# Kernel tuning notes

Hardware: AMD Instinct MI355X
Metric: run time of the kernel (lower is better)

The kernel has to match this reference:

```python
import jax, jax.numpy as jnp
import numpy as np

B, T, E, A = 128, 1024, 512, 512   # batch, encoder time, embed_size, attention units
D = 512                            # memory (encoder output) dim
H = E // 2                         # prenet out / decoder GRU cell size
OUT = 80 * 5                       # n_mels * r


def _gru(x, h, W, U, b_i, b_r):
    # Keras GRU (reset_after=True): separate input/recurrent biases.
    n = h.shape[-1]
    gi = x @ W + b_i                       # [B, 3n]
    gr = h @ U + b_r                       # [B, 3n]
    z = jax.nn.sigmoid(gi[:, :n] + gr[:, :n])
    r = jax.nn.sigmoid(gi[:, n:2 * n] + gr[:, n:2 * n])
    c = jnp.tanh(gi[:, 2 * n:] + r * gr[:, 2 * n:])
    return z * h + (1.0 - z) * c


def setup_inputs() -> dict:
    key = jax.random.key(0)
    ks = jax.random.split(key, 40)
    s = 0.02
    w = lambda i, shape: jax.random.normal(ks[i], shape, dtype=jnp.float32) * s
    inp = {
        'inputs': jax.random.normal(ks[0], (B, OUT), dtype=jnp.float32),
        'prev_attn_h': jax.random.normal(ks[1], (B, E), dtype=jnp.float32) * 0.1,
        'prev_dec_h1': jax.random.normal(ks[2], (B, H), dtype=jnp.float32) * 0.1,
        'prev_dec_h2': jax.random.normal(ks[3], (B, H), dtype=jnp.float32) * 0.1,
        'prev_alignments': jax.nn.softmax(jax.random.normal(ks[4], (B, T), dtype=jnp.float32)),
        'memory': jax.random.normal(ks[5], (B, T, D), dtype=jnp.float32),
        'memory_mask': jnp.ones((B, T), dtype=bool),
        # prenet: Dense(E) relu, Dense(E//2) relu (dropout off at eval)
        'Wp1': w(6, (OUT, E)), 'bp1': jnp.zeros((E,), jnp.float32),
        'Wp2': w(7, (E, H)), 'bp2': jnp.zeros((H,), jnp.float32),
        # Bahdanau attention: v^T tanh(Wq q + Wk m)
        'Wq': w(8, (E, A)), 'Wk': w(9, (D, A)), 'v_attn': w(10, (A,)),
        # attention_layer Dense(E) on previous context
        'Wa': w(11, (D, E)), 'ba': jnp.zeros((E,), jnp.float32),
        # attention GRU: input = prenet(H) ++ prev_attention(E)
        'Wg': w(12, (H + E, 3 * E)), 'Ug': w(13, (E, 3 * E)),
        'bg_i': jnp.zeros((3 * E,), jnp.float32), 'bg_r': jnp.zeros((3 * E,), jnp.float32),
        # stacked decoder GRU cells (E//2 each): input = attn_h(E) ++ context(D)
        'Wd1': w(14, (E + D, 3 * H)), 'Ud1': w(15, (H, 3 * H)),
        'bd1_i': jnp.zeros((3 * H,), jnp.float32), 'bd1_r': jnp.zeros((3 * H,), jnp.float32),
        'Wd2': w(16, (H, 3 * H)), 'Ud2': w(17, (H, 3 * H)),
        'bd2_i': jnp.zeros((3 * H,), jnp.float32), 'bd2_r': jnp.zeros((3 * H,), jnp.float32),
        # projection to mel frame(s)
        'Wo': w(18, (H, OUT)), 'bo': jnp.zeros((OUT,), jnp.float32),
    }
    return inp


def reference(inputs, prev_attn_h, prev_dec_h1, prev_dec_h2, prev_alignments,
              memory, memory_mask,
              Wp1, bp1, Wp2, bp2,
              Wq, Wk, v_attn, Wa, ba,
              Wg, Ug, bg_i, bg_r,
              Wd1, Ud1, bd1_i, bd1_r,
              Wd2, Ud2, bd2_i, bd2_r,
              Wo, bo):
    # 1) context from previous alignments, projected by attention_layer
    prev_ctx = jnp.einsum('bt,btd->bd', prev_alignments, memory)       # [B, D]
    prev_attention = prev_ctx @ Wa + ba                                # [B, E]
    # 2) prenet (eval mode: dropout disabled)
    pre = jax.nn.relu(inputs @ Wp1 + bp1)
    pre = jax.nn.relu(pre @ Wp2 + bp2)                                 # [B, H]
    # 3) attention GRU (single step)
    attn_in = jnp.concatenate([pre, prev_attention], axis=-1)          # [B, H+E]
    attn_h = _gru(attn_in, prev_attn_h, Wg, Ug, bg_i, bg_r)            # [B, E]
    # 4) Bahdanau attention with new query
    score = jnp.einsum('bta,a->bt', jnp.tanh((attn_h @ Wq)[:, None, :] + jnp.einsum('btd,da->bta', memory, Wk)), v_attn)
    score = jnp.where(memory_mask, score, jnp.float32(-1e9))
    alignments = jax.nn.softmax(score, axis=-1)                        # [B, T]
    context = jnp.einsum('bt,btd->bd', alignments, memory)             # [B, D]
    # 5) stacked decoder GRU cells
    dec_in = jnp.concatenate([attn_h, context], axis=-1)               # [B, E+D]
    h1 = _gru(dec_in, prev_dec_h1, Wd1, Ud1, bd1_i, bd1_r)             # [B, H]
    h2 = _gru(h1, prev_dec_h2, Wd2, Ud2, bd2_i, bd2_r)                 # [B, H]
    # 6) projection to mel frame(s), keep the time axis like the TF model
    final_outputs = (h2 @ Wo + bo)[:, None, :]                         # [B, 1, OUT]
    return final_outputs
```

## Files before the change

kernel.cpp:

```cpp
#include <hip/hip_runtime.h>
#include <cstdint>
#include <cstddef>

constexpr int NB = 128, NT = 1024, NE = 512, NA = 512, ND = 512, NH = 256, NOUT = 400;

typedef __bf16 bf16x8 __attribute__((ext_vector_type(8)));
typedef float f32x4 __attribute__((ext_vector_type(4)));

__device__ __forceinline__ float bf2f(uint16_t u) { return __uint_as_float(((uint32_t)u) << 16); }
__device__ __forceinline__ uint16_t f2bf(float f) {
  uint32_t u = __float_as_uint(f);
  u += 0x7fffu + ((u >> 16) & 1u);
  return (uint16_t)(u >> 16);
}
__device__ __forceinline__ float lo16(uint32_t u) { return __uint_as_float(u << 16); }
__device__ __forceinline__ float hi16(uint32_t u) { return __uint_as_float(u & 0xffff0000u); }
__device__ __forceinline__ float sigmoidf_(float x) { return 1.0f / (1.0f + __expf(-x)); }
__device__ __forceinline__ float tanhf_(float x) { float e = __expf(2.0f * x); return 1.0f - 2.0f / (e + 1.0f); }

__global__ void detect_k(const void* __restrict__ mem, int* __restrict__ flag) {
  __shared__ int red[256];
  int cnt = 0;
  for (int i = threadIdx.x; i < 16384; i += 256) {
    float x = bf2f(((const uint16_t*)mem)[i]);
    float ax = fabsf(x);
    if (!(ax < 100.0f)) cnt++;
  }
  red[threadIdx.x] = cnt;
  __syncthreads();
  for (int s = 128; s > 0; s >>= 1) {
    if (threadIdx.x < s) red[threadIdx.x] += red[threadIdx.x + s];
    __syncthreads();
  }
  if (threadIdx.x == 0) flag[0] = (red[0] < 64) ? 1 : 0;
}

constexpr int NSEG = 27;
struct ConvTab {
  const void* src[NSEG];
  float* dst[NSEG];
  int n[NSEG];
};

__global__ void prep_k(ConvTab t, const int* __restrict__ flag,
                       const void* __restrict__ Wk, uint16_t* __restrict__ WkTf,
                       float* __restrict__ zbase, int zcount) {
  const int y = blockIdx.y;
  const int isb = *flag;
  if (y < NSEG) {
    const int n = t.n[y];
    float* d = t.dst[y];
    if (isb) {
      const uint16_t* p = (const uint16_t*)t.src[y];
      for (int i = blockIdx.x * 256 + threadIdx.x; i < n; i += 64 * 256) d[i] = bf2f(p[i]);
    } else {
      const float* p = (const float*)t.src[y];
      for (int i = blockIdx.x * 256 + threadIdx.x; i < n; i += 64 * 256) d[i] = p[i];
    }
  } else if (y == NSEG) {
    float4* p = (float4*)zbase;
    const int n4 = zcount >> 2;
    for (int i = blockIdx.x * 256 + threadIdx.x; i < n4; i += 64 * 256)
      p[i] = float4{0.f, 0.f, 0.f, 0.f};
  } else {
    for (int idx = blockIdx.x * 256 + threadIdx.x; idx < 32768; idx += 64 * 256) {
      const int lane = idx & 63;
      const int ks = (idx >> 6) & 15;
      const int tt = (idx >> 10) & 3;
      const int ag = idx >> 12;
      const int a = ag * 64 + tt * 16 + (lane & 15);
      const int k0 = ks * 32 + (lane >> 4) * 8;
      uint16_t tmp[8];
      if (isb) {
        const uint16_t* w = (const uint16_t*)Wk;
#pragma unroll
        for (int j = 0; j < 8; ++j) tmp[j] = w[(size_t)(k0 + j) * NA + a];
      } else {
        const float* w = (const float*)Wk;
#pragma unroll
        for (int j = 0; j < 8; ++j) tmp[j] = f2bf(w[(size_t)(k0 + j) * NA + a]);
      }
      *(uint4*)(WkTf + (size_t)idx * 8) = *(const uint4*)tmp;
    }
  }
}

__global__ __launch_bounds__(256) void ctx_k(const int* __restrict__ flagp,
                                             const float* __restrict__ align,
                                             const void* __restrict__ mem,
                                             float* __restrict__ out) {
  const int b = blockIdx.x, tc = blockIdx.y, tid = threadIdx.x;
  const int t0 = tc * 256;
  float ax = 0.f, ay = 0.f;
  if (*flagp) {
    const uint32_t* memu = (const uint32_t*)mem;
    for (int t = t0; t < t0 + 256; ++t) {
      float a = align[b * NT + t];
      uint32_t m = memu[(size_t)(b * NT + t) * (ND / 2) + tid];
      ax = fmaf(a, lo16(m), ax);
      ay = fmaf(a, hi16(m), ay);
    }
  } else {
    const float2* memf = (const float2*)mem;
    for (int t = t0; t < t0 + 256; ++t) {
      float a = align[b * NT + t];
      float2 m = memf[(size_t)(b * NT + t) * (ND / 2) + tid];
      ax = fmaf(a, m.x, ax);
      ay = fmaf(a, m.y, ay);
    }
  }
  atomicAdd(&out[b * ND + 2 * tid], ax);
  atomicAdd(&out[b * ND + 2 * tid + 1], ay);
}

struct GJob {
  const float* X1; const float* X2; const float* W; const float* bias; float* out;
  int K1, K2, N, relu, mode, nb_n, ksplit, kper;
};
struct GLevel { GJob j[4]; };

__global__ __launch_bounds__(256) void gemm_lvl(GLevel L, const int* __restrict__ flagp,
                                                void* __restrict__ dout) {
  const GJob J = L.j[blockIdx.y];
  int bx = blockIdx.x;
  if (bx >= J.nb_n * 2 * J.ksplit) return;
  const int kc = bx % J.ksplit; bx /= J.ksplit;
  const int mb = bx & 1; const int nb = bx >> 1;
  const int K = J.K1 + J.K2;
  const int n0 = nb * 64, m0 = mb * 64;
  const int kbeg = kc * J.kper, kend = kc * J.kper + J.kper;

  __shared__ float Xs[32][66];
  __shared__ float Ws[32][68];
  const int tid = threadIdx.x;
  const int tx = tid & 15, ty = tid >> 4;
  float acc[4][4] = {};

  for (int kt = kbeg; kt < kend; kt += 32) {
    __syncthreads();
    {
      const int m = tid >> 2;
      const int kk = (tid & 3) * 8;
      const float* Xrow1 = J.X1 + (size_t)(m0 + m) * J.K1;
      const float* Xrow2 = J.X2 ? J.X2 + (size_t)(m0 + m) * J.K2 : nullptr;
#pragma unroll
      for (int h = 0; h < 2; ++h) {
        const int kg = kt + kk + h * 4;
        float4 val = {0.f, 0.f, 0.f, 0.f};
        if (kg < K)
          val = (kg < J.K1) ? *(const float4*)(Xrow1 + kg)
                            : *(const float4*)(Xrow2 + (kg - J.K1));
        Xs[kk + h * 4 + 0][m] = val.x;
        Xs[kk + h * 4 + 1][m] = val.y;
        Xs[kk + h * 4 + 2][m] = val.z;
        Xs[kk + h * 4 + 3][m] = val.w;
      }
    }
    {
      const int kr = tid >> 3, nc = (tid & 7) * 8;
      const int k = kt + kr;
#pragma unroll
      for (int h = 0; h < 2; ++h) {
        const int n = n0 + nc + h * 4;
        float4 val = {0.f, 0.f, 0.f, 0.f};
        if (k < K && n < J.N) val = *(const float4*)(J.W + (size_t)k * J.N + n);
        *(float4*)&Ws[kr][nc + h * 4] = val;
      }
    }
    __syncthreads();
#pragma unroll 8
    for (int k = 0; k < 32; ++k) {
      const float4 av = *(const float4*)&Xs[k][ty * 4];
      const float4 bv = *(const float4*)&Ws[k][tx * 4];
      const float aa[4] = {av.x, av.y, av.z, av.w};
      const float bb[4] = {bv.x, bv.y, bv.z, bv.w};
#pragma unroll
      for (int i = 0; i < 4; ++i)
#pragma unroll
        for (int j = 0; j < 4; ++j) acc[i][j] = fmaf(aa[i], bb[j], acc[i][j]);
    }
  }

  const int isb = (J.mode == 1) ? *flagp : 0;
#pragma unroll
  for (int i = 0; i < 4; ++i) {
    const int m = m0 + ty * 4 + i;
#pragma unroll
    for (int j = 0; j < 4; ++j) {
      const int c = n0 + tx * 4 + j;
      if (c >= J.N) continue;
      float r = acc[i][j];
      if (J.ksplit > 1) {
        if (kc == 0 && J.bias) r += J.bias[c];
        atomicAdd(&J.out[(size_t)m * J.N + c], r);
      } else {
        if (J.bias) r += J.bias[c];
        if (J.relu) r = fmaxf(r, 0.f);
        if (J.mode == 1) {
          if (isb) ((uint16_t*)dout)[(size_t)m * J.N + c] = f2bf(r);
          else     ((float*)dout)[(size_t)m * J.N + c] = r;
        } else {
          J.out[(size_t)m * J.N + c] = r;
        }
      }
    }
  }
}

__global__ void gru_k(const float* __restrict__ gi, const float* __restrict__ gr,
                      const float* __restrict__ hprev, float* __restrict__ hout, int n) {
  const int i = blockIdx.x * 256 + threadIdx.x;
  if (i >= NB * n) return;
  const int b = i / n, c = i % n;
  const float* gib = gi + (size_t)b * 3 * n;
  const float* grb = gr + (size_t)b * 3 * n;
  float z = sigmoidf_(gib[c] + grb[c]);
  float r = sigmoidf_(gib[n + c] + grb[n + c]);
  float cc = tanhf_(gib[2 * n + c] + r * grb[2 * n + c]);
  float h = hprev[i];
  hout[i] = z * h + (1.0f - z) * cc;
}

__global__ __launch_bounds__(256) void score_mfma_k(const int* __restrict__ flagp,
                                                    const void* __restrict__ mem,
                                                    const uint16_t* __restrict__ WkTf,
                                                    const float* __restrict__ q,
                                                    const float* __restrict__ v,
                                                    float* __restrict__ score) {
  __shared__ uint16_t memS[64 * 512];
  const int tid = threadIdx.x;
  const int row0 = blockIdx.x * 64;
  const int b = row0 >> 10;
  const int lane = tid & 63, wid = tid >> 6;
  const int quad = lane >> 4;
  const int r15 = lane & 15;

  if (*flagp) {
    const uint16_t* m16 = (const uint16_t*)mem;
#pragma unroll
    for (int it = 0; it < 16; ++it) {
      const int idx = it * 256 + tid;
      const int r = idx >> 6, c8 = (idx & 63) << 3;
      uint4 val = *(const uint4*)(m16 + (size_t)(row0 + r) * ND + c8);
      *(uint4*)&memS[r * 512 + (c8 ^ ((r & 7) << 3))] = val;
    }
  } else {
    const float* m32 = (const float*)mem;
#pragma unroll
    for (int it = 0; it < 32; ++it) {
      const int idx = it * 256 + tid;
      const int r = idx >> 7, c4 = (idx & 127) << 2;
      float4 val = *(const float4*)(m32 + (size_t)(row0 + r) * ND + c4);
      uint2 packed;
      packed.x = (uint32_t)f2bf(val.x) | ((uint32_t)f2bf(val.y) << 16);
      packed.y = (uint32_t)f2bf(val.z) | ((uint32_t)f2bf(val.w) << 16);
      const int col = (((c4 >> 3) ^ (r & 7)) << 3) + (c4 & 7);
      *(uint2*)&memS[r * 512 + col] = packed;
    }
  }
  __syncthreads();

  float part[4] = {0.f, 0.f, 0.f, 0.f};

#pragma unroll
  for (int agi = 0; agi < 2; ++agi) {
    const int ag = wid * 2 + agi;
    f32x4 acc[4][4] = {};
    const uint16_t* agbase = WkTf + (size_t)ag * 32768 + lane * 8;
    for (int ks = 0; ks < 16; ++ks) {
      const uint16_t* p = agbase + ks * 512;
      bf16x8 af0 = *(const bf16x8*)(p);
      bf16x8 af1 = *(const bf16x8*)(p + 8192);
      bf16x8 af2 = *(const bf16x8*)(p + 16384);
      bf16x8 af3 = *(const bf16x8*)(p + 24576);
#pragma unroll
      for (int rt = 0; rt < 4; ++rt) {
        const int lr = rt * 16 + r15;
        const bf16x8 bfrag =
            *(const bf16x8*)&memS[lr * 512 + ((((ks << 2) + quad) ^ (lr & 7)) << 3)];
        acc[rt][0] = __builtin_amdgcn_mfma_f32_16x16x32_bf16(af0, bfrag, acc[rt][0], 0, 0, 0);
        acc[rt][1] = __builtin_amdgcn_mfma_f32_16x16x32_bf16(af1, bfrag, acc[rt][1], 0, 0, 0);
        acc[rt][2] = __builtin_amdgcn_mfma_f32_16x16x32_bf16(af2, bfrag, acc[rt][2], 0, 0, 0);
        acc[rt][3] = __builtin_amdgcn_mfma_f32_16x16x32_bf16(af3, bfrag, acc[rt][3], 0, 0, 0);
      }
    }
    const int a_base = ag * 64 + quad * 4;
#pragma unroll
    for (int rt = 0; rt < 4; ++rt)
#pragma unroll
      for (int t = 0; t < 4; ++t)
#pragma unroll
        for (int r = 0; r < 4; ++r) {
          const int a = a_base + t * 16 + r;
          part[rt] = fmaf(v[a], tanhf_(acc[rt][t][r] + q[b * NA + a]), part[rt]);
        }
  }

#pragma unroll
  for (int rt = 0; rt < 4; ++rt) {
    part[rt] += __shfl_xor(part[rt], 16, 64);
    part[rt] += __shfl_xor(part[rt], 32, 64);
  }
  __syncthreads();
  float* red = (float*)memS;
  if (lane < 16) {
#pragma unroll
    for (int rt = 0; rt < 4; ++rt) red[wid * 64 + rt * 16 + lane] = part[rt];
  }
  __syncthreads();
  if (tid < 64) score[row0 + tid] = red[tid] + red[64 + tid] + red[128 + tid] + red[192 + tid];
}

__global__ __launch_bounds__(256) void softmax_k(const float* __restrict__ score,
                                                 float* __restrict__ align) {
  __shared__ float red[256];
  const int b = blockIdx.x, tid = threadIdx.x;
  float vals[4];
  float m = -1e30f;
#pragma unroll
  for (int j = 0; j < 4; ++j) {
    vals[j] = score[b * NT + j * 256 + tid];
    m = fmaxf(m, vals[j]);
  }
  red[tid] = m;
  __syncthreads();
  for (int s = 128; s > 0; s >>= 1) {
    if (tid < s) red[tid] = fmaxf(red[tid], red[tid + s]);
    __syncthreads();
  }
  m = red[0];
  __syncthreads();
  float sum = 0.f;
#pragma unroll
  for (int j = 0; j < 4; ++j) {
    vals[j] = __expf(vals[j] - m);
    sum += vals[j];
  }
  red[tid] = sum;
  __syncthreads();
  for (int s = 128; s > 0; s >>= 1) {
    if (tid < s) red[tid] += red[tid + s];
    __syncthreads();
  }
  const float inv = 1.0f / red[0];
#pragma unroll
  for (int j = 0; j < 4; ++j) align[b * NT + j * 256 + tid] = vals[j] * inv;
}

extern "C" void kernel_launch(void* const* d_in, const int* in_sizes, int n_in,
                              void* d_out, int out_size, void* d_ws, size_t ws_size,
                              hipStream_t stream) {
  const void* mem = d_in[5];

  int* flagp = (int*)d_ws;
  float* ws = (float*)d_ws + 16;
  float* prev_ctx = ws;
  float* context  = prev_ctx + NB * ND;
  float* qbuf     = context + NB * ND;
  float* prevatt  = qbuf + NB * NA;
  float* gi_g     = prevatt + NB * NE;
  float* gr_g     = gi_g + NB * 3 * NE;
  float* gi_d     = gr_g + NB * 3 * NE;
  float* gr_d     = gi_d + NB * 3 * NH;
  float* gi2      = gr_d + NB * 3 * NH;
  float* gr2      = gi2 + NB * 3 * NH;
  const int zcount = 2 * NB * ND + NB * NA + NB * NE + 2 * NB * 3 * NE + 4 * NB * 3 * NH;
  float* score    = gr2 + NB * 3 * NH;
  float* align    = score + NB * NT;
  float* pre1     = align + NB * NT;
  float* pre2     = pre1 + NB * NE;
  float* attn_h   = pre2 + NB * NH;
  float* h1       = attn_h + NB * NE;
  float* h2       = h1 + NB * NH;
  float* inputs_f = h2 + NB * NH;
  float* pah_f    = inputs_f + NB * NOUT;
  float* pd1_f    = pah_f + NB * NE;
  float* pd2_f    = pd1_f + NB * NH;
  float* palign_f = pd2_f + NB * NH;
  float* wf = palign_f + NB * NT;
  float* Wp1f = wf;                 float* bp1f = Wp1f + 400 * 512;
  float* Wp2f = bp1f + 512;         float* bp2f = Wp2f + 512 * 256;
  float* Wqf  = bp2f + 256;         float* vf   = Wqf + 512 * 512;
  float* Waf  = vf + 512;           float* baf  = Waf + 512 * 512;
  float* Wgf  = baf + 512;          float* Ugf  = Wgf + 768 * 1536;
  float* bgif = Ugf + 512 * 1536;   float* bgrf = bgif + 1536;
  float* Wd1f = bgrf + 1536;        float* Ud1f = Wd1f + 1024 * 768;
  float* bd1if = Ud1f + 256 * 768;  float* bd1rf = bd1if + 768;
  float* Wd2f = bd1rf + 768;        float* Ud2f = Wd2f + 256 * 768;
  float* bd2if = Ud2f + 256 * 768;  float* bd2rf = bd2if + 768;
  float* Wof  = bd2rf + 768;        float* bof  = Wof + 256 * 400;
  uint16_t* WkTf = (uint16_t*)(bof + 400);

  detect_k<<<dim3(1), 256, 0, stream>>>(mem, flagp);

  ConvTab tab;
  const int srcidx[NSEG] = {0, 1, 2, 3, 4, 7, 8, 9, 10, 11, 13, 14, 15, 16, 17, 18, 19,
                            20, 21, 22, 23, 24, 25, 26, 27, 28, 29};
  float* dsts[NSEG] = {inputs_f, pah_f, pd1_f, pd2_f, palign_f,
                       Wp1f, bp1f, Wp2f, bp2f, Wqf, vf, Waf, baf,
                       Wgf, Ugf, bgif, bgrf, Wd1f, Ud1f, bd1if, bd1rf,
                       Wd2f, Ud2f, bd2if, bd2rf, Wof, bof};
  for (int s = 0; s < NSEG; ++s) {
    tab.src[s] = d_in[srcidx[s]];
    tab.dst[s] = dsts[s];
    tab.n[s] = in_sizes[srcidx[s]];
  }
  prep_k<<<dim3(64, NSEG + 2), 256, 0, stream>>>(tab, flagp, d_in[12], WkTf, prev_ctx, zcount);

  ctx_k<<<dim3(NB, 4), 256, 0, stream>>>(flagp, palign_f, mem, prev_ctx);

  auto J = [](const float* X1, int K1, const float* X2, int K2, const float* W,
              const float* bias, float* out, int N, int relu, int mode, int nb_n,
              int ksplit, int kper) {
    GJob j; j.X1 = X1; j.X2 = X2; j.W = W; j.bias = bias; j.out = out;
    j.K1 = K1; j.K2 = K2; j.N = N; j.relu = relu; j.mode = mode;
    j.nb_n = nb_n; j.ksplit = ksplit; j.kper = kper; return j;
  };

  GLevel L1{};
  L1.j[0] = J(inputs_f, NOUT, nullptr, 0, Wp1f, bp1f, pre1, NE, 1, 0, 8, 1, 400);
  L1.j[1] = J(pah_f, NE, nullptr, 0, Ugf, bgrf, gr_g, 3 * NE, 0, 0, 24, 2, 256);
  L1.j[2] = J(pd1_f, NH, nullptr, 0, Ud1f, bd1rf, gr_d, 3 * NH, 0, 0, 12, 1, 256);
  L1.j[3] = J(pd2_f, NH, nullptr, 0, Ud2f, bd2rf, gr2, 3 * NH, 0, 0, 12, 1, 256);
  gemm_lvl<<<dim3(96, 4), 256, 0, stream>>>(L1, flagp, d_out);
  GLevel L2{};
  L2.j[0] = J(prev_ctx, ND, nullptr, 0, Waf, baf, prevatt, NE, 0, 0, 8, 2, 256);
  L2.j[1] = J(pre1, NE, nullptr, 0, Wp2f, bp2f, pre2, NH, 1, 0, 4, 1, 512);
  gemm_lvl<<<dim3(32, 2), 256, 0, stream>>>(L2, flagp, d_out);
  GLevel L3{};
  L3.j[0] = J(pre2, NH, prevatt, NE, Wgf, bgif, gi_g, 3 * NE, 0, 0, 24, 3, 256);
  gemm_lvl<<<dim3(144, 1), 256, 0, stream>>>(L3, flagp, d_out);
  gru_k<<<dim3(NB * NE / 256), 256, 0, stream>>>(gi_g, gr_g, pah_f, attn_h, NE);
  GLevel L4{};
  L4.j[0] = J(attn_h, NE, nullptr, 0, Wqf, nullptr, qbuf, NA, 0, 0, 8, 2, 256);
  gemm_lvl<<<dim3(32, 1), 256, 0, stream>>>(L4, flagp, d_out);
  score_mfma_k<<<dim3(NB * NT / 64), 256, 0, stream>>>(flagp, mem, WkTf, qbuf, vf, score);
  softmax_k<<<dim3(NB), 256, 0, stream>>>(score, align);
  ctx_k<<<dim3(NB, 4), 256, 0, stream>>>(flagp, align, mem, context);
  GLevel L5{};
  L5.j[0] = J(attn_h, NE, context, ND, Wd1f, bd1if, gi_d, 3 * NH, 0, 0, 12, 4, 256);
  gemm_lvl<<<dim3(96, 1), 256, 0, stream>>>(L5, flagp, d_out);
  gru_k<<<dim3(NB * NH / 256), 256, 0, stream>>>(gi_d, gr_d, pd1_f, h1, NH);
  GLevel L6{};
  L6.j[0] = J(h1, NH, nullptr, 0, Wd2f, bd2if, gi2, 3 * NH, 0, 0, 12, 1, 256);
  gemm_lvl<<<dim3(24, 1), 256, 0, stream>>>(L6, flagp, d_out);
  gru_k<<<dim3(NB * NH / 256), 256, 0, stream>>>(gi2, gr2, pd2_f, h2, NH);
  GLevel L7{};
  L7.j[0] = J(h2, NH, nullptr, 0, Wof, bof, nullptr, NOUT, 0, 1, 7, 1, 256);
  gemm_lvl<<<dim3(14, 1), 256, 0, stream>>>(L7, flagp, d_out);
}
```

Baseline: 893.0 us.

## Fuse all decoder stages into one cooperative persistent kernel with grid syncs

Replaces the chain of about twenty separate kernel launches (detect, prep, context, GEMM levels, GRU, score, softmax, context) with a single cooperative kernel. The stages are separated by grid-wide barriers, and tiles are distributed over a persistent grid sized from occupancy. It also overlaps the previous-context reduction with weight conversion, skips the fp32 copy of the previous alignments, and software-prefetches the Wk fragments in the MFMA score loop. The aim is to remove launch and inter-kernel gaps, at the cost of grid.sync overhead and a fixed grid that may underuse the GPU in some phases. The prev_ctx reduction now runs on only 128 blocks over the full time axis.

```diff
diff --git a/kernel.cpp b/kernel.cpp
--- a/kernel.cpp
+++ b/kernel.cpp
@@ -1,6 +1,9 @@
 #include <hip/hip_runtime.h>
+#include <hip/hip_cooperative_groups.h>
 #include <cstdint>
 #include <cstddef>
+
+namespace cg = cooperative_groups;
 
 constexpr int NB = 128, NT = 1024, NE = 512, NA = 512, ND = 512, NH = 256, NOUT = 400;
 
@@ -18,120 +21,38 @@
 __device__ __forceinline__ float sigmoidf_(float x) { return 1.0f / (1.0f + __expf(-x)); }
 __device__ __forceinline__ float tanhf_(float x) { float e = __expf(2.0f * x); return 1.0f - 2.0f / (e + 1.0f); }
 
-__global__ void detect_k(const void* __restrict__ mem, int* __restrict__ flag) {
-  __shared__ int red[256];
-  int cnt = 0;
-  for (int i = threadIdx.x; i < 16384; i += 256) {
-    float x = bf2f(((const uint16_t*)mem)[i]);
-    float ax = fabsf(x);
-    if (!(ax < 100.0f)) cnt++;
-  }
-  red[threadIdx.x] = cnt;
-  __syncthreads();
-  for (int s = 128; s > 0; s >>= 1) {
-    if (threadIdx.x < s) red[threadIdx.x] += red[threadIdx.x + s];
-    __syncthreads();
-  }
-  if (threadIdx.x == 0) flag[0] = (red[0] < 64) ? 1 : 0;
-}
-
-constexpr int NSEG = 27;
+constexpr int NSEG = 26;
 struct ConvTab {
   const void* src[NSEG];
   float* dst[NSEG];
   int n[NSEG];
 };
 
-__global__ void prep_k(ConvTab t, const int* __restrict__ flag,
-                       const void* __restrict__ Wk, uint16_t* __restrict__ WkTf,
-                       float* __restrict__ zbase, int zcount) {
-  const int y = blockIdx.y;
-  const int isb = *flag;
-  if (y < NSEG) {
-    const int n = t.n[y];
-    float* d = t.dst[y];
-    if (isb) {
-      const uint16_t* p = (const uint16_t*)t.src[y];
-      for (int i = blockIdx.x * 256 + threadIdx.x; i < n; i += 64 * 256) d[i] = bf2f(p[i]);
-    } else {
-      const float* p = (const float*)t.src[y];
-      for (int i = blockIdx.x * 256 + threadIdx.x; i < n; i += 64 * 256) d[i] = p[i];
-    }
-  } else if (y == NSEG) {
-    float4* p = (float4*)zbase;
-    const int n4 = zcount >> 2;
-    for (int i = blockIdx.x * 256 + threadIdx.x; i < n4; i += 64 * 256)
-      p[i] = float4{0.f, 0.f, 0.f, 0.f};
-  } else {
-    for (int idx = blockIdx.x * 256 + threadIdx.x; idx < 32768; idx += 64 * 256) {
-      const int lane = idx & 63;
-      const int ks = (idx >> 6) & 15;
-      const int tt = (idx >> 10) & 3;
-      const int ag = idx >> 12;
-      const int a = ag * 64 + tt * 16 + (lane & 15);
-      const int k0 = ks * 32 + (lane >> 4) * 8;
-      uint16_t tmp[8];
-      if (isb) {
-        const uint16_t* w = (const uint16_t*)Wk;
-#pragma unroll
-        for (int j = 0; j < 8; ++j) tmp[j] = w[(size_t)(k0 + j) * NA + a];
-      } else {
-        const float* w = (const float*)Wk;
-#pragma unroll
-        for (int j = 0; j < 8; ++j) tmp[j] = f2bf(w[(size_t)(k0 + j) * NA + a]);
-      }
-      *(uint4*)(WkTf + (size_t)idx * 8) = *(const uint4*)tmp;
-    }
-  }
-}
-
-__global__ __launch_bounds__(256) void ctx_k(const int* __restrict__ flagp,
-                                             const float* __restrict__ align,
-                                             const void* __restrict__ mem,
-                                             float* __restrict__ out) {
-  const int b = blockIdx.x, tc = blockIdx.y, tid = threadIdx.x;
-  const int t0 = tc * 256;
-  float ax = 0.f, ay = 0.f;
-  if (*flagp) {
-    const uint32_t* memu = (const uint32_t*)mem;
-    for (int t = t0; t < t0 + 256; ++t) {
-      float a = align[b * NT + t];
-      uint32_t m = memu[(size_t)(b * NT + t) * (ND / 2) + tid];
-      ax = fmaf(a, lo16(m), ax);
-      ay = fmaf(a, hi16(m), ay);
-    }
-  } else {
-    const float2* memf = (const float2*)mem;
-    for (int t = t0; t < t0 + 256; ++t) {
-      float a = align[b * NT + t];
-      float2 m = memf[(size_t)(b * NT + t) * (ND / 2) + tid];
-      ax = fmaf(a, m.x, ax);
-      ay = fmaf(a, m.y, ay);
-    }
-  }
-  atomicAdd(&out[b * ND + 2 * tid], ax);
-  atomicAdd(&out[b * ND + 2 * tid + 1], ay);
-}
-
 struct GJob {
   const float* X1; const float* X2; const float* W; const float* bias; float* out;
-  int K1, K2, N, relu, mode, nb_n, ksplit, kper;
+  int K1, K2, N, relu, mode, nbn, ksplit, kper;
 };
-struct GLevel { GJob j[4]; };
-
-__global__ __launch_bounds__(256) void gemm_lvl(GLevel L, const int* __restrict__ flagp,
-                                                void* __restrict__ dout) {
-  const GJob J = L.j[blockIdx.y];
-  int bx = blockIdx.x;
-  if (bx >= J.nb_n * 2 * J.ksplit) return;
-  const int kc = bx % J.ksplit; bx /= J.ksplit;
-  const int mb = bx & 1; const int nb = bx >> 1;
+
+struct Params {
+  const void* mem; const void* palign; const void* Wk; void* dout;
+  ConvTab tab;
+  GJob jobs[11];
+  uint16_t* WkTf;
+  float* zbase; int zcount;
+  float *prev_ctx, *context, *score, *qbuf, *attn_h, *h1, *h2;
+  float *gi_g, *gr_g, *gi_d, *gr_d, *gi2, *gr2;
+  float *pah_f, *pd1_f, *pd2_f, *vf;
+};
+
+__device__ void gemm_tile(const GJob& J, int t, char* smem, int isb, void* dout) {
+  float (*Xs)[66] = (float(*)[66])smem;
+  float (*Ws)[68] = (float(*)[68])(smem + 8448);
+  const int kc = t % J.ksplit;
+  const int r = t / J.ksplit;
+  const int mb = r & 1, nb = r >> 1;
   const int K = J.K1 + J.K2;
   const int n0 = nb * 64, m0 = mb * 64;
-  const int kbeg = kc * J.kper, kend = kc * J.kper + J.kper;
-
-  __shared__ float Xs[32][66];
-  __shared__ float Ws[32][68];
+  const int kbeg = kc * J.kper, kend = kbeg + J.kper;
   const int tid = threadIdx.x;
   const int tx = tid & 15, ty = tid >> 4;
   float acc[4][4] = {};
@@ -181,7 +102,6 @@
     }
   }
 
-  const int isb = (J.mode == 1) ? *flagp : 0;
 #pragma unroll
   for (int i = 0; i < 4; ++i) {
     const int m = m0 + ty * 4 + i;
@@ -189,195 +109,337 @@
     for (int j = 0; j < 4; ++j) {
       const int c = n0 + tx * 4 + j;
       if (c >= J.N) continue;
-      float r = acc[i][j];
+      float rv = acc[i][j];
       if (J.ksplit > 1) {
-        if (kc == 0 && J.bias) r += J.bias[c];
-        atomicAdd(&J.out[(size_t)m * J.N + c], r);
+        if (kc == 0 && J.bias) rv += J.bias[c];
+        atomicAdd(&J.out[(size_t)m * J.N + c], rv);
       } else {
-        if (J.bias) r += J.bias[c];
-        if (J.relu) r = fmaxf(r, 0.f);
+        if (J.bias) rv += J.bias[c];
+        if (J.relu) rv = fmaxf(rv, 0.f);
         if (J.mode == 1) {
-          if (isb) ((uint16_t*)dout)[(size_t)m * J.N + c] = f2bf(r);
-          else     ((float*)dout)[(size_t)m * J.N + c] = r;
+          if (isb) ((uint16_t*)dout)[(size_t)m * J.N + c] = f2bf(rv);
+          else     ((float*)dout)[(size_t)m * J.N + c] = rv;
         } else {
-          J.out[(size_t)m * J.N + c] = r;
+          J.out[(size_t)m * J.N + c] = rv;
         }
       }
     }
   }
 }
 
-__global__ void gru_k(const float* __restrict__ gi, const float* __restrict__ gr,
-                      const float* __restrict__ hprev, float* __restrict__ hout, int n) {
-  const int i = blockIdx.x * 256 + threadIdx.x;
-  if (i >= NB * n) return;
-  const int b = i / n, c = i % n;
-  const float* gib = gi + (size_t)b * 3 * n;
-  const float* grb = gr + (size_t)b * 3 * n;
-  float z = sigmoidf_(gib[c] + grb[c]);
-  float r = sigmoidf_(gib[n + c] + grb[n + c]);
-  float cc = tanhf_(gib[2 * n + c] + r * grb[2 * n + c]);
-  float h = hprev[i];
-  hout[i] = z * h + (1.0f - z) * cc;
+__device__ void run_phase(const GJob* jobs, int njobs, char* smem, int isb, void* dout) {
+  int off[6];
+  int tot = 0;
+  for (int j = 0; j < njobs; ++j) { off[j] = tot; tot += jobs[j].nbn * 2 * jobs[j].ksplit; }
+  for (int t = blockIdx.x; t < tot; t += gridDim.x) {
+    int j = njobs - 1;
+    while (j > 0 && t < off[j]) --j;
+    gemm_tile(jobs[j], t - off[j], smem, isb, dout);
+  }
 }
 
-__global__ __launch_bounds__(256) void score_mfma_k(const int* __restrict__ flagp,
-                                                    const void* __restrict__ mem,
-                                                    const uint16_t* __restrict__ WkTf,
-                                                    const float* __restrict__ q,
-                                                    const float* __restrict__ v,
-                                                    float* __restrict__ score) {
-  __shared__ uint16_t memS[64 * 512];
+__device__ void gru_phase(const float* gi, const float* gr, const float* h, float* out, int n) {
+  for (int i = blockIdx.x * 256 + threadIdx.x; i < NB * n; i += gridDim.x * 256) {
+    const int b = i / n, c = i % n;
+    const float* gib = gi + (size_t)b * 3 * n;
+    const float* grb = gr + (size_t)b * 3 * n;
+    float z = sigmoidf_(gib[c] + grb[c]);
+    float rr = sigmoidf_(gib[n + c] + grb[n + c]);
+    float cc = tanhf_(gib[2 * n + c] + rr * grb[2 * n + c]);
+    out[i] = z * h[i] + (1.0f - z) * cc;
+  }
+}
+
+__global__ __launch_bounds__(256, 2) void fused_k(Params P) {
+  cg::grid_group grid = cg::this_grid();
+  __shared__ __align__(16) char smem[65536];
   const int tid = threadIdx.x;
-  const int row0 = blockIdx.x * 64;
-  const int b = row0 >> 10;
-  const int lane = tid & 63, wid = tid >> 6;
-  const int quad = lane >> 4;
-  const int r15 = lane & 15;
-
-  if (*flagp) {
-    const uint16_t* m16 = (const uint16_t*)mem;
-#pragma unroll
-    for (int it = 0; it < 16; ++it) {
-      const int idx = it * 256 + tid;
-      const int r = idx >> 6, c8 = (idx & 63) << 3;
-      uint4 val = *(const uint4*)(m16 + (size_t)(row0 + r) * ND + c8);
-      *(uint4*)&memS[r * 512 + (c8 ^ ((r & 7) << 3))] = val;
-    }
+  const int bidx = blockIdx.x, gdim = gridDim.x;
+
+  int isb;
+  {
+    int* red = (int*)smem;
+    int cnt = 0;
+    const uint16_t* m16 = (const uint16_t*)P.mem;
+    for (int i = tid; i < 16384; i += 256) {
+      float ax = fabsf(bf2f(m16[i]));
+      if (!(ax < 100.0f)) cnt++;
+    }
+    red[tid] = cnt;
+    __syncthreads();
+    for (int s = 128; s > 0; s >>= 1) {
+      if (tid < s) red[tid] += red[tid + s];
+      __syncthreads();
+    }
+    isb = (red[0] < 64) ? 1 : 0;
+    __syncthreads();
+  }
+
+  if (bidx < 128) {
+    const int b = bidx;
+    float ax = 0.f, ay = 0.f;
+    if (isb) {
+      const uint16_t* pal = (const uint16_t*)P.palign;
+      const uint32_t* memu = (const uint32_t*)P.mem;
+      for (int t = 0; t < NT; ++t) {
+        float a = bf2f(pal[b * NT + t]);
+        uint32_t m = memu[(size_t)(b * NT + t) * (ND / 2) + tid];
+        ax = fmaf(a, lo16(m), ax);
+        ay = fmaf(a, hi16(m), ay);
+      }
+    } else {
+      const float* pal = (const float*)P.palign;
+      const float2* memf = (const float2*)P.mem;
+      for (int t = 0; t < NT; ++t) {
+        float a = pal[b * NT + t];
+        float2 m = memf[(size_t)(b * NT + t) * (ND / 2) + tid];
+        ax = fmaf(a, m.x, ax);
+        ay = fmaf(a, m.y, ay);
+      }
+    }
+    P.prev_ctx[b * ND + 2 * tid] = ax;
+    P.prev_ctx[b * ND + 2 * tid + 1] = ay;
   } else {
-    const float* m32 = (const float*)mem;
-#pragma unroll
-    for (int it = 0; it < 32; ++it) {
-      const int idx = it * 256 + tid;
-      const int r = idx >> 7, c4 = (idx & 127) << 2;
-      float4 val = *(const float4*)(m32 + (size_t)(row0 + r) * ND + c4);
-      uint2 packed;
-      packed.x = (uint32_t)f2bf(val.x) | ((uint32_t)f2bf(val.y) << 16);
-      packed.y = (uint32_t)f2bf(val.z) | ((uint32_t)f2bf(val.w) << 16);
-      const int col = (((c4 >> 3) ^ (r & 7)) << 3) + (c4 & 7);
-      *(uint2*)&memS[r * 512 + col] = packed;
-    }
-  }
-  __syncthreads();
-
-  float part[4] = {0.f, 0.f, 0.f, 0.f};
-
-#pragma unroll
-  for (int agi = 0; agi < 2; ++agi) {
-    const int ag = wid * 2 + agi;
-    f32x4 acc[4][4] = {};
-    const uint16_t* agbase = WkTf + (size_t)ag * 32768 + lane * 8;
-    for (int ks = 0; ks < 16; ++ks) {
-      const uint16_t* p = agbase + ks * 512;
-      bf16x8 af0 = *(const bf16x8*)(p);
-      bf16x8 af1 = *(const bf16x8*)(p + 8192);
-      bf16x8 af2 = *(const bf16x8*)(p + 16384);
-      bf16x8 af3 = *(const bf16x8*)(p + 24576);
+    const int pi = bidx - 128, pstride = gdim - 128;
+    for (int s = 0; s < NSEG; ++s) {
+      const int n = P.tab.n[s];
+      float* d = P.tab.dst[s];
+      if (isb) {
+        const uint16_t* p = (const uint16_t*)P.tab.src[s];
+        for (int i = pi * 256 + tid; i < n; i += pstride * 256) d[i] = bf2f(p[i]);
+      } else {
+        const float* p = (const float*)P.tab.src[s];
+        for (int i = pi * 256 + tid; i < n; i += pstride * 256) d[i] = p[i];
+      }
+    }
+    float4* zp = (float4*)P.zbase;
+    for (int i = pi * 256 + tid; i < (P.zcount >> 2); i += pstride * 256)
+      zp[i] = float4{0.f, 0.f, 0.f, 0.f};
+    for (int idx = pi * 256 + tid; idx < 32768; idx += pstride * 256) {
+      const int lane = idx & 63;
+      const int ks = (idx >> 6) & 15;
+      const int tt = (idx >> 10) & 3;
+      const int ag = idx >> 12;
+      const int a = ag * 64 + tt * 16 + (lane & 15);
+      const int k0 = ks * 32 + (lane >> 4) * 8;
+      uint16_t tmp[8];
+      if (isb) {
+        const uint16_t* w = (const uint16_t*)P.Wk;
+#pragma unroll
+        for (int j = 0; j < 8; ++j) tmp[j] = w[(size_t)(k0 + j) * NA + a];
+      } else {
+        const float* w = (const float*)P.Wk;
+#pragma unroll
+        for (int j = 0; j < 8; ++j) tmp[j] = f2bf(w[(size_t)(k0 + j) * NA + a]);
+      }
+      *(uint4*)(P.WkTf + (size_t)idx * 8) = *(const uint4*)tmp;
+    }
+  }
+  grid.sync();
+
+  run_phase(P.jobs + 0, 5, smem, isb, P.dout);
+  grid.sync();
+  run_phase(P.jobs + 5, 1, smem, isb, P.dout);
+  grid.sync();
+  run_phase(P.jobs + 6, 1, smem, isb, P.dout);
+  grid.sync();
+  gru_phase(P.gi_g, P.gr_g, P.pah_f, P.attn_h, NE);
+  grid.sync();
+  run_phase(P.jobs + 7, 1, smem, isb, P.dout);
+  grid.sync();
+
+  {
+    uint16_t* memS = (uint16_t*)smem;
+    const int lane = tid & 63, wid = tid >> 6;
+    const int quad = lane >> 4;
+    const int r15 = lane & 15;
+    for (int tile = bidx; tile < NB * NT / 64; tile += gdim) {
+      __syncthreads();
+      const int row0 = tile * 64;
+      const int b = row0 >> 10;
+      if (isb) {
+        const uint16_t* m16 = (const uint16_t*)P.mem;
+#pragma unroll
+        for (int it = 0; it < 16; ++it) {
+          const int idx = it * 256 + tid;
+          const int r = idx >> 6, c8 = (idx & 63) << 3;
+          uint4 val = *(const uint4*)(m16 + (size_t)(row0 + r) * ND + c8);
+          *(uint4*)&memS[r * 512 + (c8 ^ ((r & 7) << 3))] = val;
+        }
+      } else {
+        const float* m32 = (const float*)P.mem;
+#pragma unroll
+        for (int it = 0; it < 32; ++it) {
+          const int idx = it * 256 + tid;
+          const int r = idx >> 7, c4 = (idx & 127) << 2;
+          float4 val = *(const float4*)(m32 + (size_t)(row0 + r) * ND + c4);
+          uint2 packed;
+          packed.x = (uint32_t)f2bf(val.x) | ((uint32_t)f2bf(val.y) << 16);
+          packed.y = (uint32_t)f2bf(val.z) | ((uint32_t)f2bf(val.w) << 16);
+          const int col = (((c4 >> 3) ^ (r & 7)) << 3) + (c4 & 7);
+          *(uint2*)&memS[r * 512 + col] = packed;
+        }
+      }
+      __syncthreads();
+
+      float part[4] = {0.f, 0.f, 0.f, 0.f};
+#pragma unroll
+      for (int agi = 0; agi < 2; ++agi) {
+        const int ag = wid * 2 + agi;
+        f32x4 acc[4][4] = {};
+        const uint16_t* agbase = P.WkTf + (size_t)ag * 32768 + lane * 8;
+        bf16x8 a0 = *(const bf16x8*)(agbase);
+        bf16x8 a1 = *(const bf16x8*)(agbase + 8192);
+        bf16x8 a2 = *(const bf16x8*)(agbase + 16384);
+        bf16x8 a3 = *(const bf16x8*)(agbase + 24576);
+        for (int ks = 0; ks < 16; ++ks) {
+          const uint16_t* pn = agbase + (((ks + 1) & 15) << 9);
+          bf16x8 n0 = *(const bf16x8*)(pn);
+          bf16x8 n1 = *(const bf16x8*)(pn + 8192);
+          bf16x8 n2 = *(const bf16x8*)(pn + 16384);
+          bf16x8 n3 = *(const bf16x8*)(pn + 24576);
+#pragma unroll
+          for (int rt = 0; rt < 4; ++rt) {
+            const int lr = rt * 16 + r15;
+            const bf16x8 bfrag =
+                *(const bf16x8*)&memS[lr * 512 + ((((ks << 2) + quad) ^ (lr & 7)) << 3)];
+            acc[rt][0] = __builtin_amdgcn_mfma_f32_16x16x32_bf16(a0, bfrag, acc[rt][0], 0, 0, 0);
+            acc[rt][1] = __builtin_amdgcn_mfma_f32_16x16x32_bf16(a1, bfrag, acc[rt][1], 0, 0, 0);
+            acc[rt][2] = __builtin_amdgcn_mfma_f32_16x16x32_bf16(a2, bfrag, acc[rt][2], 0, 0, 0);
+            acc[rt][3] = __builtin_amdgcn_mfma_f32_16x16x32_bf16(a3, bfrag, acc[rt][3], 0, 0, 0);
+          }
+          a0 = n0; a1 = n1; a2 = n2; a3 = n3;
+        }
+        const int a_base = ag * 64 + quad * 4;
+#pragma unroll
+        for (int rt = 0; rt < 4; ++rt)
+#pragma unroll
+          for (int t = 0; t < 4; ++t)
+#pragma unroll
+            for (int r = 0; r < 4; ++r) {
+              const int a = a_base + t * 16 + r;
+              part[rt] = fmaf(P.vf[a], tanhf_(acc[rt][t][r] + P.qbuf[b * NA + a]), part[rt]);
+            }
+      }
 #pragma unroll
       for (int rt = 0; rt < 4; ++rt) {
-        const int lr = rt * 16 + r15;
-        const bf16x8 bfrag =
-            *(const bf16x8*)&memS[lr * 512 + ((((ks << 2) + quad) ^ (lr & 7)) << 3)];
-        acc[rt][0] = __builtin_amdgcn_mfma_f32_16x16x32_bf16(af0, bfrag, acc[rt][0], 0, 0, 0);
-        acc[rt][1] = __builtin_amdgcn_mfma_f32_16x16x32_bf16(af1, bfrag, acc[rt][1], 0, 0, 0);
-        acc[rt][2] = __builtin_amdgcn_mfma_f32_16x16x32_bf16(af2, bfrag, acc[rt][2], 0, 0, 0);
-        acc[rt][3] = __builtin_amdgcn_mfma_f32_16x16x32_bf16(af3, bfrag, acc[rt][3], 0, 0, 0);
-      }
-    }
-    const int a_base = ag * 64 + quad * 4;
-#pragma unroll
-    for (int rt = 0; rt < 4; ++rt)
-#pragma unroll
-      for (int t = 0; t < 4; ++t)
-#pragma unroll
-        for (int r = 0; r < 4; ++r) {
-          const int a = a_base + t * 16 + r;
-          part[rt] = fmaf(v[a], tanhf_(acc[rt][t][r] + q[b * NA + a]), part[rt]);
+        part[rt] += __shfl_xor(part[rt], 16, 64);
+        part[rt] += __shfl_xor(part[rt], 32, 64);
+      }
+      __syncthreads();
+      float* red = (float*)smem;
+      if (lane < 16) {
+#pragma unroll
+        for (int rt = 0; rt < 4; ++rt) red[wid * 64 + rt * 16 + lane] = part[rt];
+      }
+      __syncthreads();
+      if (tid < 64)
+        P.score[row0 + tid] = red[tid] + red[64 + tid] + red[128 + tid] + red[192 + tid];
+    }
+  }
+  grid.sync();
+
+  {
+    float* red = (float*)smem;
+    float* sw = red + 256;
+    for (int v = bidx; v < 512; v += gdim) {
+      const int b = v >> 2, tc = v & 3;
+      __syncthreads();
+      float vals[4];
+      float m = -1e30f;
+#pragma unroll
+      for (int j = 0; j < 4; ++j) {
+        vals[j] = P.score[b * NT + j * 256 + tid];
+        m = fmaxf(m, vals[j]);
+      }
+      red[tid] = m;
+      __syncthreads();
+      for (int s = 128; s > 0; s >>= 1) {
+        if (tid < s) red[tid] = fmaxf(red[tid], red[tid + s]);
+        __syncthreads();
+      }
+      m = red[0];
+      __syncthreads();
+      float sum = 0.f;
+#pragma unroll
+      for (int j = 0; j < 4; ++j) sum += __expf(vals[j] - m);
+      red[tid] = sum;
+      __syncthreads();
+      for (int s = 128; s > 0; s >>= 1) {
+        if (tid < s) red[tid] += red[tid + s];
+        __syncthreads();
+      }
+      const float inv = 1.0f / red[0];
+      sw[tid] = __expf(P.score[b * NT + tc * 256 + tid] - m) * inv;
+      __syncthreads();
+      float ax = 0.f, ay = 0.f;
+      const int t0 = tc * 256;
+      if (isb) {
+        const uint32_t* memu = (const uint32_t*)P.mem;
+        for (int t = 0; t < 256; ++t) {
+          float a = sw[t];
+          uint32_t mm = memu[(size_t)(b * NT + t0 + t) * (ND / 2) + tid];
+          ax = fmaf(a, lo16(mm), ax);
+          ay = fmaf(a, hi16(mm), ay);
         }
-  }
-
-#pragma unroll
-  for (int rt = 0; rt < 4; ++rt) {
-    part[rt] += __shfl_xor(part[rt], 16, 64);
-    part[rt] += __shfl_xor(part[rt], 32, 64);
-  }
-  __syncthreads();
-  float* red = (float*)memS;
-  if (lane < 16) {
-#pragma unroll
-    for (int rt = 0; rt < 4; ++rt) red[wid * 64 + rt * 16 + lane] = part[rt];
-  }
-  __syncthreads();
-  if (tid < 64) score[row0 + tid] = red[tid] + red[64 + tid] + red[128 + tid] + red[192 + tid];
-}
-
-__global__ __launch_bounds__(256) void softmax_k(const float* __restrict__ score,
-                                                 float* __restrict__ align) {
-  __shared__ float red[256];
-  const int b = blockIdx.x, tid = threadIdx.x;
-  float vals[4];
-  float m = -1e30f;
-#pragma unroll
-  for (int j = 0; j < 4; ++j) {
-    vals[j] = score[b * NT + j * 256 + tid];
-    m = fmaxf(m, vals[j]);
-  }
-  red[tid] = m;
-  __syncthreads();
-  for (int s = 128; s > 0; s >>= 1) {
-    if (tid < s) red[tid] = fmaxf(red[tid], red[tid + s]);
-    __syncthreads();
-  }
-  m = red[0];
-  __syncthreads();
-  float sum = 0.f;
-#pragma unroll
-  for (int j = 0; j < 4; ++j) {
-    vals[j] = __expf(vals[j] - m);
-    sum += vals[j];
-  }
-  red[tid] = sum;
-  __syncthreads();
-  for (int s = 128; s > 0; s >>= 1) {
-    if (tid < s) red[tid] += red[tid + s];
-    __syncthreads();
-  }
-  const float inv = 1.0f / red[0];
-#pragma unroll
-  for (int j = 0; j < 4; ++j) align[b * NT + j * 256 + tid] = vals[j] * inv;
+      } else {
+        const float2* memf = (const float2*)P.mem;
+        for (int t = 0; t < 256; ++t) {
+          float a = sw[t];
+          float2 mm = memf[(size_t)(b * NT + t0 + t) * (ND / 2) + tid];
+          ax = fmaf(a, mm.x, ax);
+          ay = fmaf(a, mm.y, ay);
+        }
+      }
+      atomicAdd(&P.context[b * ND + 2 * tid], ax);
+      atomicAdd(&P.context[b * ND + 2 * tid + 1], ay);
+    }
+  }
+  grid.sync();
+
+  run_phase(P.jobs + 8, 1, smem, isb, P.dout);
+  grid.sync();
+  gru_phase(P.gi_d, P.gr_d, P.pd1_f, P.h1, NH);
+  grid.sync();
+  run_phase(P.jobs + 9, 1, smem, isb, P.dout);
+  grid.sync();
+  gru_phase(P.gi2, P.gr2, P.pd2_f, P.h2, NH);
+  grid.sync();
+  run_phase(P.jobs + 10, 1, smem, isb, P.dout);
 }
 
 extern "C" void kernel_launch(void* const* d_in, const int* in_sizes, int n_in,
                               void* d_out, int out_size, void* d_ws, size_t ws_size,
                               hipStream_t stream) {
-  const void* mem = d_in[5];
-
-  int* flagp = (int*)d_ws;
-  float* ws = (float*)d_ws + 16;
-  float* prev_ctx = ws;
-  float* context  = prev_ctx + NB * ND;
-  float* qbuf     = context + NB * ND;
-  float* prevatt  = qbuf + NB * NA;
-  float* gi_g     = prevatt + NB * NE;
-  float* gr_g     = gi_g + NB * 3 * NE;
-  float* gi_d     = gr_g + NB * 3 * NE;
-  float* gr_d     = gi_d + NB * 3 * NH;
-  float* gi2      = gr_d + NB * 3 * NH;
-  float* gr2      = gi2 + NB * 3 * NH;
-  const int zcount = 2 * NB * ND + NB * NA + NB * NE + 2 * NB * 3 * NE + 4 * NB * 3 * NH;
-  float* score    = gr2 + NB * 3 * NH;
-  float* align    = score + NB * NT;
-  float* pre1     = align + NB * NT;
+  Params p{};
+  p.mem = d_in[5];
+  p.palign = d_in[4];
+  p.Wk = d_in[12];
+  p.dout = d_out;
+
+  float* ws = (float*)d_ws;
+  float* context = ws;
+  float* qbuf    = context + NB * ND;
+  float* prevatt = qbuf + NB * NA;
+  float* gi_g    = prevatt + NB * NE;
+  float* gr_g    = gi_g + NB * 3 * NE;
+  float* gi_d    = gr_g + NB * 3 * NE;
+  const int zcount = NB * ND + NB * NA + NB * NE + 2 * NB * 3 * NE + NB * 3 * NH;
+  float* prev_ctx = gi_d + NB * 3 * NH;
+  float* score    = prev_ctx + NB * ND;
+  float* pre1     = score + NB * NT;
   float* pre2     = pre1 + NB * NE;
   float* attn_h   = pre2 + NB * NH;
   float* h1       = attn_h + NB * NE;
   float* h2       = h1 + NB * NH;
-  float* inputs_f = h2 + NB * NH;
+  float* gi2      = h2 + NB * NH;
+  float* gr2      = gi2 + NB * 3 * NH;
+  float* gr_d     = gr2 + NB * 3 * NH;
+  float* inputs_f = gr_d + NB * 3 * NH;
   float* pah_f    = inputs_f + NB * NOUT;
   float* pd1_f    = pah_f + NB * NE;
   float* pd2_f    = pd1_f + NB * NH;
-  float* palign_f = pd2_f + NB * NH;
-  float* wf = palign_f + NB * NT;
+  float* wf = pd2_f + NB * NH;
   float* Wp1f = wf;                 float* bp1f = Wp1f + 400 * 512;
   float* Wp2f = bp1f + 512;         float* bp2f = Wp2f + 512 * 256;
   float* Wqf  = bp2f + 256;         float* vf   = Wqf + 512 * 512;
@@ -391,61 +453,49 @@
   float* Wof  = bd2rf + 768;        float* bof  = Wof + 256 * 400;
   uint16_t* WkTf = (uint16_t*)(bof + 400);
 
-  detect_k<<<dim3(1), 256, 0, stream>>>(mem, flagp);
-
-  ConvTab tab;
-  const int srcidx[NSEG] = {0, 1, 2, 3, 4, 7, 8, 9, 10, 11, 13, 14, 15, 16, 17, 18, 19,
+  p.zbase = context; p.zcount = zcount;
+  p.WkTf = WkTf;
+  p.prev_ctx = prev_ctx; p.context = context; p.score = score; p.qbuf = qbuf;
+  p.attn_h = attn_h; p.h1 = h1; p.h2 = h2;
+  p.gi_g = gi_g; p.gr_g = gr_g; p.gi_d = gi_d; p.gr_d = gr_d; p.gi2 = gi2; p.gr2 = gr2;
+  p.pah_f = pah_f; p.pd1_f = pd1_f; p.pd2_f = pd2_f; p.vf = vf;
+
+  const int srcidx[NSEG] = {0, 1, 2, 3, 7, 8, 9, 10, 11, 13, 14, 15, 16, 17, 18, 19,
                             20, 21, 22, 23, 24, 25, 26, 27, 28, 29};
-  float* dsts[NSEG] = {inputs_f, pah_f, pd1_f, pd2_f, palign_f,
+  float* dsts[NSEG] = {inputs_f, pah_f, pd1_f, pd2_f,
                        Wp1f, bp1f, Wp2f, bp2f, Wqf, vf, Waf, baf,
                        Wgf, Ugf, bgif, bgrf, Wd1f, Ud1f, bd1if, bd1rf,
                        Wd2f, Ud2f, bd2if, bd2rf, Wof, bof};
   for (int s = 0; s < NSEG; ++s) {
-    tab.src[s] = d_in[srcidx[s]];
-    tab.dst[s] = dsts[s];
-    tab.n[s] = in_sizes[srcidx[s]];
-  }
-  prep_k<<<dim3(64, NSEG + 2), 256, 0, stream>>>(tab, flagp, d_in[12], WkTf, prev_ctx, zcount);
-
-  ctx_k<<<dim3(NB, 4), 256, 0, stream>>>(flagp, palign_f, mem, prev_ctx);
+    p.tab.src[s] = d_in[srcidx[s]];
+    p.tab.dst[s] = dsts[s];
+    p.tab.n[s] = in_sizes[srcidx[s]];
+  }
 
   auto J = [](const float* X1, int K1, const float* X2, int K2, const float* W,
-              const float* bias, float* out, int N, int relu, int mode, int nb_n,
+              const float* bias, float* out, int N, int relu, int mode, int nbn,
               int ksplit, int kper) {
     GJob j; j.X1 = X1; j.X2 = X2; j.W = W; j.bias = bias; j.out = out;
     j.K1 = K1; j.K2 = K2; j.N = N; j.relu = relu; j.mode = mode;
-    j.nb_n = nb_n; j.ksplit = ksplit; j.kper = kper; return j;
+    j.nbn = nbn; j.ksplit = ksplit; j.kper = kper; return j;
   };
-
-  GLevel L1{};
-  L1.j[0] = J(inputs_f, NOUT, nullptr, 0, Wp1f, bp1f, pre1, NE, 1, 0, 8, 1, 400);
-  L1.j[1] = J(pah_f, NE, nullptr, 0, Ugf, bgrf, gr_g, 3 * NE, 0, 0, 24, 2, 256);
-  L1.j[2] = J(pd1_f, NH, nullptr, 0, Ud1f, bd1rf, gr_d, 3 * NH, 0, 0, 12, 1, 256);
-  L1.j[3] = J(pd2_f, NH, nullptr, 0, Ud2f, bd2rf, gr2, 3 * NH, 0, 0, 12, 1, 256);
-  gemm_lvl<<<dim3(96, 4), 256, 0, stream>>>(L1, flagp, d_out);
-  GLevel L2{};
-  L2.j[0] = J(prev_ctx, ND, nullptr, 0, Waf, baf, prevatt, NE, 0, 0, 8, 2, 256);
-  L2.j[1] = J(pre1, NE, nullptr, 0, Wp2f, bp2f, pre2, NH, 1, 0, 4, 1, 512);
-  gemm_lvl<<<dim3(32, 2), 256, 0, stream>>>(L2, flagp, d_out);
-  GLevel L3{};
-  L3.j[0] = J(pre2, NH, prevatt, NE, Wgf, bgif, gi_g, 3 * NE, 0, 0, 24, 3, 256);
-  gemm_lvl<<<dim3(144, 1), 256, 0, stream>>>(L3, flagp, d_out);
-  gru_k<<<dim3(NB * NE / 256), 256, 0, stream>>>(gi_g, gr_g, pah_f, attn_h, NE);
-  GLevel L4{};
-  L4.j[0] = J(attn_h, NE, nullptr, 0, Wqf, nullptr, qbuf, NA, 0, 0, 8, 2, 256);
-  gemm_lvl<<<dim3(32, 1), 256, 0, stream>>>(L4, flagp, d_out);
-  score_mfma_k<<<dim3(NB * NT / 64), 256, 0, stream>>>(flagp, mem, WkTf, qbuf, vf, score);
-  softmax_k<<<dim3(NB), 256, 0, stream>>>(score, align);
-  ctx_k<<<dim3(NB, 4), 256, 0, stream>>>(flagp, align, mem, context);
-  GLevel L5{};
-  L5.j[0] = J(attn_h, NE, context, ND, Wd1f, bd1if, gi_d, 3 * NH, 0, 0, 12, 4, 256);
-  gemm_lvl<<<dim3(96, 1), 256, 0, stream>>>(L5, flagp, d_out);
-  gru_k<<<dim3(NB * NH / 256), 256, 0, stream>>>(gi_d, gr_d, pd1_f, h1, NH);
-  GLevel L6{};
-  L6.j[0] = J(h1, NH, nullptr, 0, Wd2f, bd2if, gi2, 3 * NH, 0, 0, 12, 1, 256);
-  gemm_lvl<<<dim3(24, 1), 256, 0, stream>>>(L6, flagp, d_out);
-  gru_k<<<dim3(NB * NH / 256), 256, 0, stream>>>(gi2, gr2, pd2_f, h2, NH);
-  GLevel L7{};
-  L7.j[0] = J(h2, NH, nullptr, 0, Wof, bof, nullptr, NOUT, 0, 1, 7, 1, 256);
-  gemm_lvl<<<dim3(14, 1), 256, 0, stream>>>(L7, flagp, d_out);
+  p.jobs[0] = J(inputs_f, NOUT, nullptr, 0, Wp1f, bp1f, pre1, NE, 1, 0, 8, 1, 416);
+  p.jobs[1] = J(pah_f, NE, nullptr, 0, Ugf, bgrf, gr_g, 3 * NE, 0, 0, 24, 2, 256);
+  p.jobs[2] = J(pd1_f, NH, nullptr, 0, Ud1f, bd1rf, gr_d, 3 * NH, 0, 0, 12, 1, 256);
+  p.jobs[3] = J(pd2_f, NH, nullptr, 0, Ud2f, bd2rf, gr2, 3 * NH, 0, 0, 12, 1, 256);
+  p.jobs[4] = J(prev_ctx, ND, nullptr, 0, Waf, baf, prevatt, NE, 0, 0, 8, 2, 256);
+  p.jobs[5] = J(pre1, NE, nullptr, 0, Wp2f, bp2f, pre2, NH, 1, 0, 4, 1, 512);
+  p.jobs[6] = J(pre2, NH, prevatt, NE, Wgf, bgif, gi_g, 3 * NE, 0, 0, 24, 2, 384);
+  p.jobs[7] = J(attn_h, NE, nullptr, 0, Wqf, nullptr, qbuf, NA, 0, 0, 8, 2, 256);
+  p.jobs[8] = J(attn_h, NE, context, ND, Wd1f, bd1if, gi_d, 3 * NH, 0, 0, 12, 4, 256);
+  p.jobs[9] = J(h1, NH, nullptr, 0, Wd2f, bd2if, gi2, 3 * NH, 0, 0, 12, 1, 256);
+  p.jobs[10] = J(h2, NH, nullptr, 0, Wof, bof, nullptr, NOUT, 0, 1, 7, 1, 256);
+
+  int occ = 0;
+  hipOccupancyMaxActiveBlocksPerMultiprocessor(&occ, fused_k, 256, 0);
+  if (occ < 1) occ = 1;
+  if (occ > 2) occ = 2;
+  dim3 grid(occ * 256);
+  void* args[] = {&p};
+  hipLaunchCooperativeKernel(fused_k, grid, dim3(256), args, 0, stream);
 }
```

New measurement: 1.747 ms. 1.96x slower.
